# Kernel tuning notes

Hardware: AMD Instinct MI355X
Metric: run time of the kernel (lower is better)

Reference implementation:

```python
import jax, jax.numpy as jnp
import numpy as np

STATE_LEN, SEQ_LEN, HIDDEN = 2048, 4096, 2048

def setup_inputs() -> dict:
    key = jax.random.key(0)
    k1, k2, k3, k4 = jax.random.split(key, 4)
    scale = 1.0 / np.sqrt(HIDDEN)
    return {
        "out_state": jax.random.normal(k1, (STATE_LEN, HIDDEN), dtype=jnp.float32),
        "history": jax.random.normal(k2, (SEQ_LEN, HIDDEN), dtype=jnp.float32),
        "W": jax.random.normal(k3, (HIDDEN, HIDDEN), dtype=jnp.float32) * scale,
        "b": jax.random.normal(k4, (HIDDEN,), dtype=jnp.float32) * scale,
    }

def reference(out_state, history, W, b):
    # method='general': energy_j = Linear(history_j) = history_j @ W.T + b
    # score[i, j] = out_state_i . energy_j  -> batched GEMM replacing the double loop
    energies = history @ W.T + b                 # [seq_len, hidden]
    scores = jnp.einsum('ih,jh->ij', out_state, energies)  # [state_len, seq_len]
    # F.softmax on a 2D tensor (legacy default) normalizes over dim=1 (rows)
    return jax.nn.softmax(scores, axis=-1)
```

## Files before the change

### kernel.cpp

```cpp
#include <hip/hip_runtime.h>


#define STATE_LEN 2048
#define SEQ_LEN   4096
#define HIDDEN    2048

#define BM 128
#define BK 32

typedef __bf16 bf16x8 __attribute__((ext_vector_type(8)));
typedef float f32x4 __attribute__((ext_vector_type(4)));

__device__ __forceinline__ unsigned short f32_to_bf16(float f) {
  unsigned u = __float_as_uint(f);
  u += 0x7FFFu + ((u >> 16) & 1u);
  return (unsigned short)(u >> 16);
}
__device__ __forceinline__ float bf16_to_f32(unsigned short h) {
  return __uint_as_float(((unsigned)h) << 16);
}

__device__ __forceinline__ void gld16(const void* g, void* l) {
  __builtin_amdgcn_global_load_lds(
      (const __attribute__((address_space(1))) unsigned int*)g,
      (__attribute__((address_space(3))) unsigned int*)l,
      16, 0, 0);
}

__global__ __launch_bounds__(256) void split_kernel(
    const float* __restrict__ in, unsigned short* __restrict__ hi,
    unsigned short* __restrict__ lo, int n) {
  int i = (blockIdx.x * 256 + threadIdx.x) * 4;
  if (i >= n) return;
  float4 v = *(const float4*)&in[i];
  ushort4 h, l;
  h.x = f32_to_bf16(v.x); l.x = f32_to_bf16(v.x - bf16_to_f32(h.x));
  h.y = f32_to_bf16(v.y); l.y = f32_to_bf16(v.y - bf16_to_f32(h.y));
  h.z = f32_to_bf16(v.z); l.z = f32_to_bf16(v.z - bf16_to_f32(h.z));
  h.w = f32_to_bf16(v.w); l.w = f32_to_bf16(v.w - bf16_to_f32(h.w));
  *(ushort4*)&hi[i] = h;
  *(ushort4*)&lo[i] = l;
}

__global__ __launch_bounds__(256) void transpose_split_kernel(
    const float* __restrict__ in, unsigned short* __restrict__ hi,
    unsigned short* __restrict__ lo, int rows, int cols) {
  __shared__ float tile[32][33];
  const int bx = blockIdx.x * 32;
  const int by = blockIdx.y * 32;
  const int tx = threadIdx.x;
  const int ty = threadIdx.y;
#pragma unroll
  for (int i = 0; i < 32; i += 8)
    tile[ty + i][tx] = in[(size_t)(by + ty + i) * cols + (bx + tx)];
  __syncthreads();
#pragma unroll
  for (int i = 0; i < 32; i += 8) {
    float x = tile[tx][ty + i];
    unsigned short h = f32_to_bf16(x);
    unsigned short l = f32_to_bf16(x - bf16_to_f32(h));
    size_t o = (size_t)(bx + ty + i) * rows + (by + tx);
    hi[o] = h;
    lo[o] = l;
  }
}

__global__ __launch_bounds__(256) void reduce_split(
    const float* __restrict__ p0, const float* __restrict__ p1,
    unsigned short* __restrict__ hi, unsigned short* __restrict__ lo, int n) {
  int i = (blockIdx.x * 256 + threadIdx.x) * 4;
  if (i >= n) return;
  float4 a = *(const float4*)&p0[i];
  float4 b = *(const float4*)&p1[i];
  a.x += b.x; a.y += b.y; a.z += b.z; a.w += b.w;
  ushort4 h, l;
  h.x = f32_to_bf16(a.x); l.x = f32_to_bf16(a.x - bf16_to_f32(h.x));
  h.y = f32_to_bf16(a.y); l.y = f32_to_bf16(a.y - bf16_to_f32(h.y));
  h.z = f32_to_bf16(a.z); l.z = f32_to_bf16(a.z - bf16_to_f32(h.z));
  h.w = f32_to_bf16(a.w); l.w = f32_to_bf16(a.w - bf16_to_f32(h.w));
  *(ushort4*)&hi[i] = h;
  *(ushort4*)&lo[i] = l;
}

template <int BN, bool SPLIT_OUT, int KSPLIT>
__global__ __launch_bounds__(256, 2) void gemm_bt_split(
    const unsigned short* __restrict__ Ahi, const unsigned short* __restrict__ Alo,
    const unsigned short* __restrict__ Bhi, const unsigned short* __restrict__ Blo,
    float* __restrict__ Cf, unsigned short* __restrict__ Chi,
    unsigned short* __restrict__ Clo, int M, int N, int K) {
  constexpr int NI = BN / 32;
  __shared__ __align__(16) unsigned short sAhi[BM * BK];
  __shared__ __align__(16) unsigned short sAlo[BM * BK];
  __shared__ __align__(16) unsigned short sBhi[BN * BK];
  __shared__ __align__(16) unsigned short sBlo[BN * BK];

  const int t = threadIdx.x;
  const int tileM = blockIdx.y * BM;
  const int tileN = blockIdx.x * BN;
  const int kBase = (KSPLIT > 1) ? blockIdx.z * (K / KSPLIT) : 0;
  const int kEnd = kBase + K / KSPLIT;
  if (KSPLIT > 1) Cf += (size_t)blockIdx.z * M * N;
  const int rr = t >> 2;
  const int cc = t & 3;

  const int lane = t & 63;
  const int wave = t >> 6;
  const int wm = wave >> 1;
  const int wn = wave & 1;
  const int lr = lane & 15;
  const int kqc = lane >> 4;

  f32x4 acc[4][NI] = {};

  for (int k0 = kBase; k0 < kEnd; k0 += BK) {
#pragma unroll
    for (int it = 0; it < 2; ++it) {
      const int r = it * 64 + rr;
      const int q = cc ^ ((r >> 1) & 3);
      const size_t ga = (size_t)(tileM + r) * K + k0 + q * 8;
      const int ls = r * BK + cc * 8;
      gld16(Ahi + ga, &sAhi[ls]);
      gld16(Alo + ga, &sAlo[ls]);
    }
#pragma unroll
    for (int it = 0; it < BN / 64; ++it) {
      const int r = it * 64 + rr;
      const int q = cc ^ ((r >> 1) & 3);
      const size_t gb = (size_t)(tileN + r) * K + k0 + q * 8;
      const int ls = r * BK + cc * 8;
      gld16(Bhi + gb, &sBhi[ls]);
      gld16(Blo + gb, &sBlo[ls]);
    }
    __syncthreads();

    bf16x8 ah[4], al[4], bh[NI], bl[NI];
#pragma unroll
    for (int mi = 0; mi < 4; ++mi) {
      const int R = wm * 64 + mi * 16 + lr;
      const int off = R * BK + (kqc ^ ((R >> 1) & 3)) * 8;
      ah[mi] = *(const bf16x8*)&sAhi[off];
      al[mi] = *(const bf16x8*)&sAlo[off];
    }
#pragma unroll
    for (int ni = 0; ni < NI; ++ni) {
      const int R = wn * (BN / 2) + ni * 16 + lr;
      const int off = R * BK + (kqc ^ ((R >> 1) & 3)) * 8;
      bh[ni] = *(const bf16x8*)&sBhi[off];
      bl[ni] = *(const bf16x8*)&sBlo[off];
    }
#pragma unroll
    for (int mi = 0; mi < 4; ++mi)
#pragma unroll
      for (int ni = 0; ni < NI; ++ni) {
        acc[mi][ni] = __builtin_amdgcn_mfma_f32_16x16x32_bf16(ah[mi], bh[ni], acc[mi][ni], 0, 0, 0);
        acc[mi][ni] = __builtin_amdgcn_mfma_f32_16x16x32_bf16(ah[mi], bl[ni], acc[mi][ni], 0, 0, 0);
        acc[mi][ni] = __builtin_amdgcn_mfma_f32_16x16x32_bf16(al[mi], bh[ni], acc[mi][ni], 0, 0, 0);
      }
    __syncthreads();
  }

#pragma unroll
  for (int mi = 0; mi < 4; ++mi)
#pragma unroll
    for (int ni = 0; ni < NI; ++ni)
#pragma unroll
      for (int e = 0; e < 4; ++e) {
        const int row = tileM + wm * 64 + mi * 16 + (lane >> 4) * 4 + e;
        const int col = tileN + wn * (BN / 2) + ni * 16 + lr;
        const float x = acc[mi][ni][e];
        const size_t o = (size_t)row * N + col;
        if (SPLIT_OUT) {
          const unsigned short h = f32_to_bf16(x);
          Chi[o] = h;
          Clo[o] = f32_to_bf16(x - bf16_to_f32(h));
        } else {
          Cf[o] = x;
        }
      }
}

__global__ __launch_bounds__(256) void softmax_rows(float* __restrict__ d, int cols) {
  const int row = blockIdx.x;
  float* p = d + (size_t)row * cols;
  const int t = threadIdx.x;
  const int lane = t & 63;
  const int wave = t >> 6;
  __shared__ float sred[4];

  float4 v[4];
  float m = -3.0e38f;
#pragma unroll
  for (int k = 0; k < 4; ++k) {
    v[k] = *(float4*)&p[(t + k * 256) * 4];
    m = fmaxf(m, fmaxf(fmaxf(v[k].x, v[k].y), fmaxf(v[k].z, v[k].w)));
  }
#pragma unroll
  for (int off = 32; off > 0; off >>= 1) m = fmaxf(m, __shfl_xor(m, off, 64));
  if (lane == 0) sred[wave] = m;
  __syncthreads();
  m = fmaxf(fmaxf(sred[0], sred[1]), fmaxf(sred[2], sred[3]));
  __syncthreads();

  float s = 0.f;
#pragma unroll
  for (int k = 0; k < 4; ++k) {
    v[k].x = __expf(v[k].x - m);
    v[k].y = __expf(v[k].y - m);
    v[k].z = __expf(v[k].z - m);
    v[k].w = __expf(v[k].w - m);
    s += (v[k].x + v[k].y) + (v[k].z + v[k].w);
  }
#pragma unroll
  for (int off = 32; off > 0; off >>= 1) s += __shfl_xor(s, off, 64);
  if (lane == 0) sred[wave] = s;
  __syncthreads();
  s = (sred[0] + sred[1]) + (sred[2] + sred[3]);
  const float inv = 1.0f / s;
#pragma unroll
  for (int k = 0; k < 4; ++k) {
    v[k].x *= inv; v[k].y *= inv; v[k].z *= inv; v[k].w *= inv;
    *(float4*)&p[(t + k * 256) * 4] = v[k];
  }
}

extern "C" void kernel_launch(void* const* d_in, const int* in_sizes, int n_in,
                              void* d_out, int out_size, void* d_ws, size_t ws_size,
                              hipStream_t stream) {
  const float* out_state = (const float*)d_in[0];
  const float* history   = (const float*)d_in[1];
  const float* W         = (const float*)d_in[2];
  float* out = (float*)d_out;

  char* ws = (char*)d_ws;
  const size_t MB = 1ull << 20;
  unsigned short* ohi  = (unsigned short*)(ws + 0 * MB);
  unsigned short* olo  = (unsigned short*)(ws + 8 * MB);
  unsigned short* wthi = (unsigned short*)(ws + 16 * MB);
  unsigned short* wtlo = (unsigned short*)(ws + 24 * MB);
  unsigned short* hhi  = (unsigned short*)(ws + 32 * MB);
  unsigned short* hlo  = (unsigned short*)(ws + 48 * MB);
  float*          part = (float*)(ws + 64 * MB);
  unsigned short* thi  = (unsigned short*)(ws + 16 * MB);
  unsigned short* tlo  = (unsigned short*)(ws + 24 * MB);

  split_kernel<<<(STATE_LEN * HIDDEN) / 1024, 256, 0, stream>>>(out_state, ohi, olo,
                                                                STATE_LEN * HIDDEN);
  transpose_split_kernel<<<dim3(HIDDEN / 32, HIDDEN / 32), dim3(32, 8), 0, stream>>>(
      W, wthi, wtlo, HIDDEN, HIDDEN);
  split_kernel<<<(SEQ_LEN * HIDDEN) / 1024, 256, 0, stream>>>(history, hhi, hlo,
                                                              SEQ_LEN * HIDDEN);
  gemm_bt_split<128, false, 2>
      <<<dim3(HIDDEN / 128, STATE_LEN / 128, 2), 256, 0, stream>>>(
          ohi, olo, wthi, wtlo, part, nullptr, nullptr, STATE_LEN, HIDDEN, HIDDEN);
  reduce_split<<<(STATE_LEN * HIDDEN) / 1024, 256, 0, stream>>>(
      part, part + (size_t)STATE_LEN * HIDDEN, thi, tlo, STATE_LEN * HIDDEN);
  gemm_bt_split<128, false, 1>
      <<<dim3(SEQ_LEN / 128, STATE_LEN / 128), 256, 0, stream>>>(
          thi, tlo, hhi, hlo, out, nullptr, nullptr, STATE_LEN, SEQ_LEN, HIDDEN);
  softmax_rows<<<STATE_LEN, 256, 0, stream>>>(out, SEQ_LEN);
}
```

Measured before the change: 280.7 us.

## Split-K both GEMMs and fuse second reduction into softmax

The first GEMM goes from 2-way to 4-way split-K, with two of its partial buffers placed in the output buffer. The second GEMM becomes 2-way split-K, and its two partials are summed inside the softmax kernel, so no separate reduction pass is needed. Launch bounds rise to 4 blocks per SM. The goal is more concurrent blocks on MI355X's many CUs; the cost is extra partial-sum memory traffic and possibly register spilling under the tighter occupancy bound.

```diff
diff --git a/kernel.cpp b/kernel.cpp
--- a/kernel.cpp
+++ b/kernel.cpp
@@ -65,14 +65,20 @@
   }
 }
 
-__global__ __launch_bounds__(256) void reduce_split(
+__global__ __launch_bounds__(256) void reduce_split4(
     const float* __restrict__ p0, const float* __restrict__ p1,
+    const float* __restrict__ p2, const float* __restrict__ p3,
     unsigned short* __restrict__ hi, unsigned short* __restrict__ lo, int n) {
   int i = (blockIdx.x * 256 + threadIdx.x) * 4;
   if (i >= n) return;
   float4 a = *(const float4*)&p0[i];
   float4 b = *(const float4*)&p1[i];
-  a.x += b.x; a.y += b.y; a.z += b.z; a.w += b.w;
+  float4 c = *(const float4*)&p2[i];
+  float4 d = *(const float4*)&p3[i];
+  a.x = (a.x + b.x) + (c.x + d.x);
+  a.y = (a.y + b.y) + (c.y + d.y);
+  a.z = (a.z + b.z) + (c.z + d.z);
+  a.w = (a.w + b.w) + (c.w + d.w);
   ushort4 h, l;
   h.x = f32_to_bf16(a.x); l.x = f32_to_bf16(a.x - bf16_to_f32(h.x));
   h.y = f32_to_bf16(a.y); l.y = f32_to_bf16(a.y - bf16_to_f32(h.y));
@@ -82,12 +88,12 @@
   *(ushort4*)&lo[i] = l;
 }
 
-template <int BN, bool SPLIT_OUT, int KSPLIT>
-__global__ __launch_bounds__(256, 2) void gemm_bt_split(
+template <int BN, int KSPLIT>
+__global__ __launch_bounds__(256, 4) void gemm_bt_split(
     const unsigned short* __restrict__ Ahi, const unsigned short* __restrict__ Alo,
     const unsigned short* __restrict__ Bhi, const unsigned short* __restrict__ Blo,
-    float* __restrict__ Cf, unsigned short* __restrict__ Chi,
-    unsigned short* __restrict__ Clo, int M, int N, int K) {
+    float* __restrict__ Cf0, float* __restrict__ Cf1,
+    float* __restrict__ Cf2, float* __restrict__ Cf3, int M, int N, int K) {
   constexpr int NI = BN / 32;
   __shared__ __align__(16) unsigned short sAhi[BM * BK];
   __shared__ __align__(16) unsigned short sAlo[BM * BK];
@@ -97,9 +103,15 @@
   const int t = threadIdx.x;
   const int tileM = blockIdx.y * BM;
   const int tileN = blockIdx.x * BN;
-  const int kBase = (KSPLIT > 1) ? blockIdx.z * (K / KSPLIT) : 0;
+  const int z = (KSPLIT > 1) ? blockIdx.z : 0;
+  const int kBase = z * (K / KSPLIT);
   const int kEnd = kBase + K / KSPLIT;
-  if (KSPLIT > 1) Cf += (size_t)blockIdx.z * M * N;
+  float* Cf = Cf0;
+  if (KSPLIT > 1) {
+    if (z == 1) Cf = Cf1;
+    else if (z == 2) Cf = Cf2;
+    else if (z == 3) Cf = Cf3;
+  }
   const int rr = t >> 2;
   const int cc = t & 3;
 
@@ -167,21 +179,16 @@
       for (int e = 0; e < 4; ++e) {
         const int row = tileM + wm * 64 + mi * 16 + (lane >> 4) * 4 + e;
         const int col = tileN + wn * (BN / 2) + ni * 16 + lr;
-        const float x = acc[mi][ni][e];
-        const size_t o = (size_t)row * N + col;
-        if (SPLIT_OUT) {
-          const unsigned short h = f32_to_bf16(x);
-          Chi[o] = h;
-          Clo[o] = f32_to_bf16(x - bf16_to_f32(h));
-        } else {
-          Cf[o] = x;
-        }
+        Cf[(size_t)row * N + col] = acc[mi][ni][e];
       }
 }
 
-__global__ __launch_bounds__(256) void softmax_rows(float* __restrict__ d, int cols) {
+__global__ __launch_bounds__(256) void reduce_softmax(float* __restrict__ d,
+                                                      const float* __restrict__ part,
+                                                      int cols) {
   const int row = blockIdx.x;
   float* p = d + (size_t)row * cols;
+  const float* q = part + (size_t)row * cols;
   const int t = threadIdx.x;
   const int lane = t & 63;
   const int wave = t >> 6;
@@ -191,8 +198,11 @@
   float m = -3.0e38f;
 #pragma unroll
   for (int k = 0; k < 4; ++k) {
-    v[k] = *(float4*)&p[(t + k * 256) * 4];
-    m = fmaxf(m, fmaxf(fmaxf(v[k].x, v[k].y), fmaxf(v[k].z, v[k].w)));
+    float4 a = *(const float4*)&p[(t + k * 256) * 4];
+    float4 b = *(const float4*)&q[(t + k * 256) * 4];
+    a.x += b.x; a.y += b.y; a.z += b.z; a.w += b.w;
+    v[k] = a;
+    m = fmaxf(m, fmaxf(fmaxf(a.x, a.y), fmaxf(a.z, a.w)));
   }
 #pragma unroll
   for (int off = 32; off > 0; off >>= 1) m = fmaxf(m, __shfl_xor(m, off, 64));
@@ -239,9 +249,13 @@
   unsigned short* wtlo = (unsigned short*)(ws + 24 * MB);
   unsigned short* hhi  = (unsigned short*)(ws + 32 * MB);
   unsigned short* hlo  = (unsigned short*)(ws + 48 * MB);
-  float*          part = (float*)(ws + 64 * MB);
-  unsigned short* thi  = (unsigned short*)(ws + 16 * MB);
-  unsigned short* tlo  = (unsigned short*)(ws + 24 * MB);
+  float*          pws  = (float*)(ws + 64 * MB);
+  float* g1p0 = pws;
+  float* g1p1 = pws + (size_t)STATE_LEN * HIDDEN;
+  float* g1p2 = out;
+  float* g1p3 = out + (size_t)STATE_LEN * HIDDEN;
+  unsigned short* thi = (unsigned short*)(ws + 0 * MB);
+  unsigned short* tlo = (unsigned short*)(ws + 8 * MB);
 
   split_kernel<<<(STATE_LEN * HIDDEN) / 1024, 256, 0, stream>>>(out_state, ohi, olo,
                                                                 STATE_LEN * HIDDEN);
@@ -249,13 +263,13 @@
       W, wthi, wtlo, HIDDEN, HIDDEN);
   split_kernel<<<(SEQ_LEN * HIDDEN) / 1024, 256, 0, stream>>>(history, hhi, hlo,
                                                               SEQ_LEN * HIDDEN);
-  gemm_bt_split<128, false, 2>
-      <<<dim3(HIDDEN / 128, STATE_LEN / 128, 2), 256, 0, stream>>>(
-          ohi, olo, wthi, wtlo, part, nullptr, nullptr, STATE_LEN, HIDDEN, HIDDEN);
-  reduce_split<<<(STATE_LEN * HIDDEN) / 1024, 256, 0, stream>>>(
-      part, part + (size_t)STATE_LEN * HIDDEN, thi, tlo, STATE_LEN * HIDDEN);
-  gemm_bt_split<128, false, 1>
-      <<<dim3(SEQ_LEN / 128, STATE_LEN / 128), 256, 0, stream>>>(
-          thi, tlo, hhi, hlo, out, nullptr, nullptr, STATE_LEN, SEQ_LEN, HIDDEN);
-  softmax_rows<<<STATE_LEN, 256, 0, stream>>>(out, SEQ_LEN);
-}
+  gemm_bt_split<128, 4>
+      <<<dim3(HIDDEN / 128, STATE_LEN / 128, 4), 256, 0, stream>>>(
+          ohi, olo, wthi, wtlo, g1p0, g1p1, g1p2, g1p3, STATE_LEN, HIDDEN, HIDDEN);
+  reduce_split4<<<(STATE_LEN * HIDDEN) / 1024, 256, 0, stream>>>(
+      g1p0, g1p1, g1p2, g1p3, thi, tlo, STATE_LEN * HIDDEN);
+  gemm_bt_split<128, 2>
+      <<<dim3(SEQ_LEN / 128, STATE_LEN / 128, 2), 256, 0, stream>>>(
+          thi, tlo, hhi, hlo, out, pws, nullptr, nullptr, STATE_LEN, SEQ_LEN, HIDDEN);
+  reduce_softmax<<<STATE_LEN, 256, 0, stream>>>(out, pws, SEQ_LEN);
+}
```

New measurement: 298.4 us. +6.3%, slower.
